# Performance work log

Hardware: AMD Instinct MI355X
Metric: run time of the kernel (lower is better)

Reference implementation:

```python
import jax, jax.numpy as jnp
import numpy as np

B, C, H, W = 2, 256, 32, 32
PK, CK = 256, 256


def setup_inputs() -> dict:
    key = jax.random.key(0)
    ks = jax.random.split(key, 9)
    s = 1.0 / np.sqrt(C)
    return {
        'x': jax.random.normal(ks[0], (B, C, H, W), jnp.float32),
        'primary_indices': jax.random.randint(ks[1], (B, PK), 0, B * H * W),
        'compare_indices': jax.random.randint(ks[2], (B, CK), 0, B * H * W),
        'pre_w': jax.random.uniform(ks[3], (3, C, C), jnp.float32, -s, s),
        'pre_b': jax.random.uniform(ks[4], (3, C), jnp.float32, -s, s),
        'post_w': jax.random.uniform(ks[5], (2, C, C), jnp.float32, -s, s),
        'post_b': jax.random.uniform(ks[6], (2, C), jnp.float32, -s, s),
        'post_out_w': jax.random.uniform(ks[7], (2, C), jnp.float32, -s, s),
        'post_out_b': jax.random.uniform(ks[8], (2,), jnp.float32, -s, s),
    }


def reference(x, primary_indices, compare_indices, pre_w, pre_b,
              post_w, post_b, post_out_w, post_out_b):
    # pre_compare: stack of 1x1 convs (c->c->c->c), ReLU between layers
    h = x
    for i in range(3):
        h = jnp.einsum('bchw,oc->bohw', h, pre_w[i]) + pre_b[i][None, :, None, None]
        if i < 2:
            h = jax.nn.relu(h)
    bs, c, hh, ww = h.shape
    # flatten to [bs*h*w, c] node features (matches torch transpose+reshape)
    flat = h.reshape(bs, c, hh * ww).transpose(0, 2, 1).reshape(bs * hh * ww, c)
    # gather primary / compare node features with global flat indices
    xp = flat[primary_indices.reshape(-1)].reshape(bs, -1, c).transpose(0, 2, 1)  # [b,c,pk]
    xc = flat[compare_indices.reshape(-1)].reshape(bs, -1, c).transpose(0, 2, 1)  # [b,c,ck]
    # broadcast pairwise squared difference -> [b,c,pk,ck]
    xx = (xp[:, :, :, None] - xc[:, :, None, :]) ** 2
    # post_compare: 1x1 conv stack c->c->c->2, ReLU between layers
    g = xx
    for i in range(2):
        g = jax.nn.relu(jnp.einsum('bcpq,oc->bopq', g, post_w[i]) + post_b[i][None, :, None, None])
    out = jnp.einsum('bcpq,oc->bopq', g, post_out_w) + post_out_b[None, :, None, None]
    return out  # [b, 2, pk, ck]
```

## Files before the change

### kernel.cpp

```cpp
#include <hip/hip_runtime.h>

typedef unsigned short u16;
typedef short bf16x8 __attribute__((ext_vector_type(8)));
typedef float f32x4 __attribute__((ext_vector_type(4)));
typedef u16 u16x4 __attribute__((ext_vector_type(4)));

__device__ __forceinline__ float b2f(u16 h) {
  unsigned u = ((unsigned)h) << 16;
  return __builtin_bit_cast(float, u);
}
__device__ __forceinline__ u16 f2b(float f) {
  return __builtin_bit_cast(u16, (__bf16)f);
}
__device__ __forceinline__ void gld_lds16(const void* g, void* l) {
  __builtin_amdgcn_global_load_lds(
      (__attribute__((address_space(1))) void*)(g),
      (__attribute__((address_space(3))) void*)(l), 16, 0, 0);
}

__global__ void dense_edge_prep(const float* __restrict__ x,
                                const float* __restrict__ pre_w,
                                const float* __restrict__ post_w,
                                u16* __restrict__ wb, u16* __restrict__ xt) {
  const int blk = blockIdx.x;
  const int t = threadIdx.x;
  if (blk < 160) {
    const int id = blk * 256 + t;
    const int layer = id >> 13;
    const int sid = id & 8191;
    const int m = sid >> 5;
    const int s8 = sid & 31;
    const float* src = (layer < 2) ? (post_w + layer * 65536)
                                   : (pre_w + (layer - 2) * 65536);
    u16* dst = wb + layer * 65536;
    f32x4 a = *(const f32x4*)(src + m * 256 + s8 * 8);
    f32x4 c = *(const f32x4*)(src + m * 256 + s8 * 8 + 4);
    bf16x8 o;
#pragma unroll
    for (int j = 0; j < 4; j++) o[j] = (short)f2b(a[j]);
#pragma unroll
    for (int j = 0; j < 4; j++) o[4 + j] = (short)f2b(c[j]);
    *(bf16x8*)(dst + (s8 * 256 + m) * 8) = o;
  } else {
    __shared__ float tile[32 * 65];
    const int xb = blk - 160;
    const int b = xb >> 7;
    const int ct = (xb >> 4) & 7;
    const int ht = xb & 15;
    const int c0 = ct * 32, hw0 = ht * 64;
#pragma unroll
    for (int rep = 0; rep < 8; rep++) {
      const int idx = rep * 256 + t;
      const int cl = idx >> 6, hl = idx & 63;
      tile[cl * 65 + hl] = x[(b * 256 + c0 + cl) * 1024 + hw0 + hl];
    }
    __syncthreads();
    const int hl = t >> 2, c8 = t & 3;
    bf16x8 o;
#pragma unroll
    for (int i = 0; i < 8; i++) o[i] = (short)f2b(tile[(c8 * 8 + i) * 65 + hl]);
    *(bf16x8*)(xt + (b * 1024 + hw0 + hl) * 256 + c0 + c8 * 8) = o;
  }
}

__global__ __launch_bounds__(256, 2) void dense_edge_pre(
    const u16* __restrict__ xt, const u16* __restrict__ wpre,
    const float* __restrict__ preb, u16* __restrict__ flat) {
  __shared__ u16 feat[2][2112];
  const int t = threadIdx.x;
  const int wv = t >> 6, ln = t & 63;
  const int nb = blockIdx.x * 8;
  const int q4 = ln >> 4, r15 = ln & 15;

  {
    const int s8 = t >> 3, nl = t & 7;
    gld_lds16(xt + (nb + nl) * 256 + s8 * 8, &feat[0][t * 8]);
  }
  __syncthreads();

#pragma unroll
  for (int l = 0; l < 3; l++) {
    const u16* wl = wpre + l * 65536;
    f32x4 acc[4];
    f32x4 zero = {0.f, 0.f, 0.f, 0.f};
#pragma unroll
    for (int mt = 0; mt < 4; mt++) acc[mt] = zero;
#pragma unroll
    for (int s = 0; s < 8; s++) {
      bf16x8 bv = *(const bf16x8*)(&feat[l & 1][((s * 4 + q4) * 8 + r15) * 8]);
#pragma unroll
      for (int mt = 0; mt < 4; mt++) {
        bf16x8 av = *(const bf16x8*)(wl + ((s * 4 + q4) * 256 + wv * 64 + mt * 16 + r15) * 8);
        acc[mt] = __builtin_amdgcn_mfma_f32_16x16x32_bf16(av, bv, acc[mt], 0, 0, 0);
      }
    }
    if (l < 2) {
#pragma unroll
      for (int mt = 0; mt < 4; mt++) {
        const int o = wv * 64 + mt * 16 + q4 * 4;
        f32x4 bb = *(const f32x4*)(preb + l * 256 + o);
        u16x4 pk;
#pragma unroll
        for (int r = 0; r < 4; r++) {
          float v = fmaxf(acc[mt][r] + bb[r], 0.f);
          pk[r] = f2b(v);
        }
        if (r15 < 8)
          *(u16x4*)(&feat[(l + 1) & 1][((o >> 3) * 8 + r15) * 8 + (o & 7)]) = pk;
      }
      __syncthreads();
    } else {
#pragma unroll
      for (int mt = 0; mt < 4; mt++) {
        const int o = wv * 64 + mt * 16 + q4 * 4;
        f32x4 bb = *(const f32x4*)(preb + 512 + o);
        u16x4 pk;
#pragma unroll
        for (int r = 0; r < 4; r++) pk[r] = f2b(acc[mt][r] + bb[r]);
        if (r15 < 8) *(u16x4*)(flat + (nb + r15) * 256 + o) = pk;
      }
    }
  }
}

#define NT 8
__global__ __launch_bounds__(512, 2) void dense_edge_main(
    const u16* __restrict__ flat, const int* __restrict__ pidx,
    const int* __restrict__ cidx, const u16* __restrict__ w1s,
    const u16* __restrict__ w2s, const float* __restrict__ b1,
    const float* __restrict__ b2, const float* __restrict__ w3,
    const float* __restrict__ b3, float* __restrict__ out) {
  __shared__ u16 xxbuf[2][16384];
  __shared__ u16 t1buf[2][16384];
  __shared__ u16 pstage[2048];
  __shared__ u16 qstage[2][2048];
  __shared__ float pbuf[2][8][2][64];

  const int t = threadIdx.x;
  const int wv = t >> 6;
  const int ln = t & 63;
  const int q4 = ln >> 4, r15 = ln & 15;
  const int blk = blockIdx.x;
  const int tile0 = blk * NT;
  const int b = tile0 >> 10;
  const int pt = (tile0 >> 5) & 31;
  const int qt0 = tile0 & 31;
  const int p0 = pt * 8;

  bf16x8 w1f[2][8], w2f[2][8];
#pragma unroll
  for (int s = 0; s < 8; s++)
#pragma unroll
    for (int mt = 0; mt < 2; mt++) {
      const int off = ((s * 4 + q4) * 256 + wv * 32 + mt * 16 + r15) * 8;
      w1f[mt][s] = *(const bf16x8*)(w1s + off);
      w2f[mt][s] = *(const bf16x8*)(w2s + off);
    }

  const int slot4 = (wv & 3) * 64 + ln;
  const int srow = slot4 & 7, scc = slot4 >> 3;
  if (wv < 4) {
    const int pn = pidx[b * 256 + p0 + srow];
    gld_lds16(flat + pn * 256 + scc * 8, &pstage[slot4 * 8]);
  } else {
    const int qn = cidx[b * 256 + qt0 * 8 + srow];
    gld_lds16(flat + qn * 256 + scc * 8, &qstage[0][slot4 * 8]);
  }
  int qn_pro = 0, qn_cur = 0;
  if (wv >= 4) {
    qn_pro = cidx[b * 256 + (qt0 + 1) * 8 + srow];
    qn_cur = cidx[b * 256 + (qt0 + 2) * 8 + srow];
  }
  __syncthreads();

  const int prow = ln >> 3, qrow = ln & 7;

  bf16x8 pa[4];
#pragma unroll
  for (int i = 0; i < 4; i++)
    pa[i] = *(const bf16x8*)(&pstage[((wv * 4 + i) * 8 + prow) * 8]);

  auto do_xx = [&](int jx) {
    const u16* qs = qstage[jx & 1];
    u16* xb = xxbuf[jx & 1];
#pragma unroll
    for (int i = 0; i < 4; i++) {
      const int cc = wv * 4 + i;
      bf16x8 av = pa[i];
      bf16x8 bv = *(const bf16x8*)(&qs[(cc * 8 + qrow) * 8]);
      bf16x8 ov;
#pragma unroll
      for (int jj = 0; jj < 8; jj++) {
        float d = b2f((u16)av[jj]) - b2f((u16)bv[jj]);
        ov[jj] = (short)f2b(d * d);
      }
      *(bf16x8*)(&xb[(cc * 64 + ln) * 8]) = ov;
    }
  };

  auto do_g1 = [&](int jg) {
    const u16* xb = xxbuf[jg & 1];
    f32x4 acc[2][4];
    {
      f32x4 zero = {0.f, 0.f, 0.f, 0.f};
#pragma unroll
      for (int mt = 0; mt < 2; mt++)
#pragma unroll
        for (int nt = 0; nt < 4; nt++) acc[mt][nt] = zero;
    }
    __builtin_amdgcn_s_setprio(1);
#pragma unroll
    for (int s = 0; s < 8; s++) {
      bf16x8 bfr[4];
#pragma unroll
      for (int nt = 0; nt < 4; nt++)
        bfr[nt] = *(const bf16x8*)(xb + ((s * 4 + q4) * 64 + nt * 16 + r15) * 8);
#pragma unroll
      for (int mt = 0; mt < 2; mt++)
#pragma unroll
        for (int nt = 0; nt < 4; nt++)
          acc[mt][nt] = __builtin_amdgcn_mfma_f32_16x16x32_bf16(w1f[mt][s], bfr[nt], acc[mt][nt], 0, 0, 0);
    }
    __builtin_amdgcn_s_setprio(0);
#pragma unroll
    for (int mt = 0; mt < 2; mt++) {
      const int o = wv * 32 + mt * 16 + q4 * 4;
      f32x4 bb = *(const f32x4*)(b1 + o);
#pragma unroll
      for (int nt = 0; nt < 4; nt++) {
        const int nn = nt * 16 + r15;
        u16x4 pk;
#pragma unroll
        for (int r = 0; r < 4; r++) {
          float v = fmaxf(acc[mt][nt][r] + bb[r], 0.f);
          pk[r] = f2b(v);
        }
        *(u16x4*)(&t1buf[jg & 1][((o >> 3) * 64 + nn) * 8 + (o & 7)]) = pk;
      }
    }
  };

  auto do_g2 = [&](int jg) {
    const u16* tb = t1buf[jg & 1];
    f32x4 acc[2][4];
    {
      f32x4 zero = {0.f, 0.f, 0.f, 0.f};
#pragma unroll
      for (int mt = 0; mt < 2; mt++)
#pragma unroll
        for (int nt = 0; nt < 4; nt++) acc[mt][nt] = zero;
    }
    __builtin_amdgcn_s_setprio(1);
#pragma unroll
    for (int s = 0; s < 8; s++) {
      bf16x8 bfr[4];
#pragma unroll
      for (int nt = 0; nt < 4; nt++)
        bfr[nt] = *(const bf16x8*)(tb + ((s * 4 + q4) * 64 + nt * 16 + r15) * 8);
#pragma unroll
      for (int mt = 0; mt < 2; mt++)
#pragma unroll
        for (int nt = 0; nt < 4; nt++)
          acc[mt][nt] = __builtin_amdgcn_mfma_f32_16x16x32_bf16(w2f[mt][s], bfr[nt], acc[mt][nt], 0, 0, 0);
    }
    __builtin_amdgcn_s_setprio(0);
    float part[2][4] = {{0.f, 0.f, 0.f, 0.f}, {0.f, 0.f, 0.f, 0.f}};
#pragma unroll
    for (int mt = 0; mt < 2; mt++) {
      const int o = wv * 32 + mt * 16 + q4 * 4;
      f32x4 bb = *(const f32x4*)(b2 + o);
      f32x4 w3a = *(const f32x4*)(w3 + o);
      f32x4 w3b = *(const f32x4*)(w3 + 256 + o);
#pragma unroll
      for (int nt = 0; nt < 4; nt++) {
#pragma unroll
        for (int r = 0; r < 4; r++) {
          float v = fmaxf(acc[mt][nt][r] + bb[r], 0.f);
          part[0][nt] += v * w3a[r];
          part[1][nt] += v * w3b[r];
        }
      }
    }
#pragma unroll
    for (int o3 = 0; o3 < 2; o3++)
#pragma unroll
      for (int nt = 0; nt < 4; nt++) {
        part[o3][nt] += __shfl_xor(part[o3][nt], 16, 64);
        part[o3][nt] += __shfl_xor(part[o3][nt], 32, 64);
      }
    if (q4 == 0) {
#pragma unroll
      for (int o3 = 0; o3 < 2; o3++)
#pragma unroll
        for (int nt = 0; nt < 4; nt++)
          pbuf[jg & 1][wv][o3][nt * 16 + r15] = part[o3][nt];
    }
  };

  do_xx(0);
  if (wv >= 4) gld_lds16(flat + qn_pro * 256 + scc * 8, &qstage[1][slot4 * 8]);
  __syncthreads();

#pragma unroll 1
  for (int j = 0; j <= NT; j++) {
    if (j >= 2 && t < 128) {
      const int jo = j - 2;
      const int o3 = t >> 6;
      const int n = t & 63;
      float v = b3[o3];
#pragma unroll
      for (int k = 0; k < 8; k++) v += pbuf[jo & 1][k][o3][n];
      out[((b * 2 + o3) * 256 + p0 + (n >> 3)) * 256 + (qt0 + jo) * 8 + (n & 7)] = v;
    }
    if (j < NT - 2 && wv >= 4) {
      gld_lds16(flat + qn_cur * 256 + scc * 8, &qstage[j & 1][slot4 * 8]);
      if (j < NT - 3) qn_cur = cidx[b * 256 + (qt0 + j + 3) * 8 + srow];
    }
    if (wv & 4) {
      if (j < NT - 1) do_xx(j + 1);
      if (j > 0) do_g2(j - 1);
      if (j < NT) do_g1(j);
    } else {
      if (j < NT) do_g1(j);
      if (j > 0) do_g2(j - 1);
      if (j < NT - 1) do_xx(j + 1);
    }
    __syncthreads();
  }

  if (t < 128) {
    const int jo = NT - 1;
    const int o3 = t >> 6;
    const int n = t & 63;
    float v = b3[o3];
#pragma unroll
    for (int k = 0; k < 8; k++) v += pbuf[jo & 1][k][o3][n];
    out[((b * 2 + o3) * 256 + p0 + (n >> 3)) * 256 + (qt0 + jo) * 8 + (n & 7)] = v;
  }
}

extern "C" void kernel_launch(void* const* d_in, const int* in_sizes, int n_in,
                              void* d_out, int out_size, void* d_ws, size_t ws_size,
                              hipStream_t stream) {
  (void)in_sizes; (void)n_in; (void)out_size; (void)ws_size;
  const float* x          = (const float*)d_in[0];
  const int*   pidx       = (const int*)d_in[1];
  const int*   cidx       = (const int*)d_in[2];
  const float* pre_w      = (const float*)d_in[3];
  const float* pre_b      = (const float*)d_in[4];
  const float* post_w     = (const float*)d_in[5];
  const float* post_b     = (const float*)d_in[6];
  const float* post_out_w = (const float*)d_in[7];
  const float* post_out_b = (const float*)d_in[8];
  float* out = (float*)d_out;

  u16* ws   = (u16*)d_ws;
  u16* wb   = ws;
  u16* w1s  = wb;
  u16* w2s  = wb + 65536;
  u16* wpre = wb + 131072;
  u16* xt   = ws + 327680;
  u16* flat = ws + 851968;

  dense_edge_prep<<<416, 256, 0, stream>>>(x, pre_w, post_w, wb, xt);
  dense_edge_pre<<<256, 256, 0, stream>>>(xt, wpre, pre_b, flat);
  dense_edge_main<<<256, 512, 0, stream>>>(flat, pidx, cidx, w1s, w2s,
                                           post_b, post_b + 256,
                                           post_out_w, post_out_b, out);
}
```

Measured before the change: 119.6 us.

## Specialize waves into layer-1 producers and layer-2 consumers with per-layer weight registers

Splits the eight waves into two groups. Four producer waves compute the squared differences and the first post-conv GEMM. The other four consumer waves run the second GEMM, the output reduction and the global stores. Each wave now holds only one layer's weights, covering 64 output channels instead of 32 per layer. This halves the weight register footprint per output and removes duplicate weight loading across layers. The trade-off is possible load imbalance between the groups, since the producer waves also do the xx computation, and more accumulator registers per wave.

```diff
diff --git a/kernel.cpp b/kernel.cpp
--- a/kernel.cpp
+++ b/kernel.cpp
@@ -134,12 +134,14 @@
   __shared__ u16 t1buf[2][16384];
   __shared__ u16 pstage[2048];
   __shared__ u16 qstage[2][2048];
-  __shared__ float pbuf[2][8][2][64];
+  __shared__ float pbuf[2][4][2][64];
 
   const int t = threadIdx.x;
   const int wv = t >> 6;
   const int ln = t & 63;
   const int q4 = ln >> 4, r15 = ln & 15;
+  const bool prod = wv < 4;
+  const int cw = wv & 3;
   const int blk = blockIdx.x;
   const int tile0 = blk * NT;
   const int b = tile0 >> 10;
@@ -147,46 +149,37 @@
   const int qt0 = tile0 & 31;
   const int p0 = pt * 8;
 
-  bf16x8 w1f[2][8], w2f[2][8];
+  const u16* wsrc = prod ? w1s : w2s;
+  bf16x8 af_w[4][8];
 #pragma unroll
   for (int s = 0; s < 8; s++)
 #pragma unroll
-    for (int mt = 0; mt < 2; mt++) {
-      const int off = ((s * 4 + q4) * 256 + wv * 32 + mt * 16 + r15) * 8;
-      w1f[mt][s] = *(const bf16x8*)(w1s + off);
-      w2f[mt][s] = *(const bf16x8*)(w2s + off);
-    }
-
-  const int slot4 = (wv & 3) * 64 + ln;
+    for (int mt = 0; mt < 4; mt++)
+      af_w[mt][s] = *(const bf16x8*)(wsrc + ((s * 4 + q4) * 256 + cw * 64 + mt * 16 + r15) * 8);
+
+  const int slot4 = cw * 64 + ln;
   const int srow = slot4 & 7, scc = slot4 >> 3;
-  if (wv < 4) {
+  int qn_pro = 0, qn_cur = 0;
+  if (prod) {
     const int pn = pidx[b * 256 + p0 + srow];
     gld_lds16(flat + pn * 256 + scc * 8, &pstage[slot4 * 8]);
+    qn_pro = cidx[b * 256 + (qt0 + 1) * 8 + srow];
+    qn_cur = cidx[b * 256 + (qt0 + 2) * 8 + srow];
   } else {
     const int qn = cidx[b * 256 + qt0 * 8 + srow];
     gld_lds16(flat + qn * 256 + scc * 8, &qstage[0][slot4 * 8]);
   }
-  int qn_pro = 0, qn_cur = 0;
-  if (wv >= 4) {
-    qn_pro = cidx[b * 256 + (qt0 + 1) * 8 + srow];
-    qn_cur = cidx[b * 256 + (qt0 + 2) * 8 + srow];
-  }
   __syncthreads();
 
   const int prow = ln >> 3, qrow = ln & 7;
-
-  bf16x8 pa[4];
-#pragma unroll
-  for (int i = 0; i < 4; i++)
-    pa[i] = *(const bf16x8*)(&pstage[((wv * 4 + i) * 8 + prow) * 8]);
 
   auto do_xx = [&](int jx) {
     const u16* qs = qstage[jx & 1];
     u16* xb = xxbuf[jx & 1];
 #pragma unroll
-    for (int i = 0; i < 4; i++) {
-      const int cc = wv * 4 + i;
-      bf16x8 av = pa[i];
+    for (int i = 0; i < 8; i++) {
+      const int cc = cw * 8 + i;
+      bf16x8 av = *(const bf16x8*)(&pstage[(cc * 8 + prow) * 8]);
       bf16x8 bv = *(const bf16x8*)(&qs[(cc * 8 + qrow) * 8]);
       bf16x8 ov;
 #pragma unroll
@@ -200,11 +193,11 @@
 
   auto do_g1 = [&](int jg) {
     const u16* xb = xxbuf[jg & 1];
-    f32x4 acc[2][4];
+    f32x4 acc[4][4];
     {
       f32x4 zero = {0.f, 0.f, 0.f, 0.f};
 #pragma unroll
-      for (int mt = 0; mt < 2; mt++)
+      for (int mt = 0; mt < 4; mt++)
 #pragma unroll
         for (int nt = 0; nt < 4; nt++) acc[mt][nt] = zero;
     }
@@ -216,15 +209,15 @@
       for (int nt = 0; nt < 4; nt++)
         bfr[nt] = *(const bf16x8*)(xb + ((s * 4 + q4) * 64 + nt * 16 + r15) * 8);
 #pragma unroll
-      for (int mt = 0; mt < 2; mt++)
+      for (int mt = 0; mt < 4; mt++)
 #pragma unroll
         for (int nt = 0; nt < 4; nt++)
-          acc[mt][nt] = __builtin_amdgcn_mfma_f32_16x16x32_bf16(w1f[mt][s], bfr[nt], acc[mt][nt], 0, 0, 0);
+          acc[mt][nt] = __builtin_amdgcn_mfma_f32_16x16x32_bf16(af_w[mt][s], bfr[nt], acc[mt][nt], 0, 0, 0);
     }
     __builtin_amdgcn_s_setprio(0);
 #pragma unroll
-    for (int mt = 0; mt < 2; mt++) {
-      const int o = wv * 32 + mt * 16 + q4 * 4;
+    for (int mt = 0; mt < 4; mt++) {
+      const int o = cw * 64 + mt * 16 + q4 * 4;
       f32x4 bb = *(const f32x4*)(b1 + o);
 #pragma unroll
       for (int nt = 0; nt < 4; nt++) {
@@ -242,11 +235,11 @@
 
   auto do_g2 = [&](int jg) {
     const u16* tb = t1buf[jg & 1];
-    f32x4 acc[2][4];
+    f32x4 acc[4][4];
     {
       f32x4 zero = {0.f, 0.f, 0.f, 0.f};
 #pragma unroll
-      for (int mt = 0; mt < 2; mt++)
+      for (int mt = 0; mt < 4; mt++)
 #pragma unroll
         for (int nt = 0; nt < 4; nt++) acc[mt][nt] = zero;
     }
@@ -258,16 +251,16 @@
       for (int nt = 0; nt < 4; nt++)
         bfr[nt] = *(const bf16x8*)(tb + ((s * 4 + q4) * 64 + nt * 16 + r15) * 8);
 #pragma unroll
-      for (int mt = 0; mt < 2; mt++)
+      for (int mt = 0; mt < 4; mt++)
 #pragma unroll
         for (int nt = 0; nt < 4; nt++)
-          acc[mt][nt] = __builtin_amdgcn_mfma_f32_16x16x32_bf16(w2f[mt][s], bfr[nt], acc[mt][nt], 0, 0, 0);
+          acc[mt][nt] = __builtin_amdgcn_mfma_f32_16x16x32_bf16(af_w[mt][s], bfr[nt], acc[mt][nt], 0, 0, 0);
     }
     __builtin_amdgcn_s_setprio(0);
     float part[2][4] = {{0.f, 0.f, 0.f, 0.f}, {0.f, 0.f, 0.f, 0.f}};
 #pragma unroll
-    for (int mt = 0; mt < 2; mt++) {
-      const int o = wv * 32 + mt * 16 + q4 * 4;
+    for (int mt = 0; mt < 4; mt++) {
+      const int o = cw * 64 + mt * 16 + q4 * 4;
       f32x4 bb = *(const f32x4*)(b2 + o);
       f32x4 w3a = *(const f32x4*)(w3 + o);
       f32x4 w3b = *(const f32x4*)(w3 + 256 + o);
@@ -293,49 +286,54 @@
       for (int o3 = 0; o3 < 2; o3++)
 #pragma unroll
         for (int nt = 0; nt < 4; nt++)
-          pbuf[jg & 1][wv][o3][nt * 16 + r15] = part[o3][nt];
+          pbuf[jg & 1][cw][o3][nt * 16 + r15] = part[o3][nt];
     }
   };
 
-  do_xx(0);
-  if (wv >= 4) gld_lds16(flat + qn_pro * 256 + scc * 8, &qstage[1][slot4 * 8]);
+  if (prod) {
+    do_xx(0);
+    gld_lds16(flat + qn_pro * 256 + scc * 8, &qstage[1][slot4 * 8]);
+  }
   __syncthreads();
 
 #pragma unroll 1
   for (int j = 0; j <= NT; j++) {
-    if (j >= 2 && t < 128) {
-      const int jo = j - 2;
-      const int o3 = t >> 6;
-      const int n = t & 63;
+    if (prod) {
+      if (j < NT - 2) {
+        gld_lds16(flat + qn_cur * 256 + scc * 8, &qstage[j & 1][slot4 * 8]);
+        if (j < NT - 3) qn_cur = cidx[b * 256 + (qt0 + j + 3) * 8 + srow];
+      }
+      if (j < NT) do_g1(j);
+      if (j < NT - 1) do_xx(j + 1);
+    } else {
+      if (j >= 2) {
+        const int jo = j - 2;
+        const int tt = t & 255;
+        if (tt < 128) {
+          const int o3 = tt >> 6;
+          const int n = tt & 63;
+          float v = b3[o3];
+#pragma unroll
+          for (int k = 0; k < 4; k++) v += pbuf[jo & 1][k][o3][n];
+          out[((b * 2 + o3) * 256 + p0 + (n >> 3)) * 256 + (qt0 + jo) * 8 + (n & 7)] = v;
+        }
+      }
+      if (j > 0) do_g2(j - 1);
+    }
+    __syncthreads();
+  }
+
+  if (!prod) {
+    const int jo = NT - 1;
+    const int tt = t & 255;
+    if (tt < 128) {
+      const int o3 = tt >> 6;
+      const int n = tt & 63;
       float v = b3[o3];
 #pragma unroll
-      for (int k = 0; k < 8; k++) v += pbuf[jo & 1][k][o3][n];
+      for (int k = 0; k < 4; k++) v += pbuf[jo & 1][k][o3][n];
       out[((b * 2 + o3) * 256 + p0 + (n >> 3)) * 256 + (qt0 + jo) * 8 + (n & 7)] = v;
     }
-    if (j < NT - 2 && wv >= 4) {
-      gld_lds16(flat + qn_cur * 256 + scc * 8, &qstage[j & 1][slot4 * 8]);
-      if (j < NT - 3) qn_cur = cidx[b * 256 + (qt0 + j + 3) * 8 + srow];
-    }
-    if (wv & 4) {
-      if (j < NT - 1) do_xx(j + 1);
-      if (j > 0) do_g2(j - 1);
-      if (j < NT) do_g1(j);
-    } else {
-      if (j < NT) do_g1(j);
-      if (j > 0) do_g2(j - 1);
-      if (j < NT - 1) do_xx(j + 1);
-    }
-    __syncthreads();
-  }
-
-  if (t < 128) {
-    const int jo = NT - 1;
-    const int o3 = t >> 6;
-    const int n = t & 63;
-    float v = b3[o3];
-#pragma unroll
-    for (int k = 0; k < 8; k++) v += pbuf[jo & 1][k][o3][n];
-    out[((b * 2 + o3) * 256 + p0 + (n >> 3)) * 256 + (qt0 + jo) * 8 + (n & 7)] = v;
   }
 }
 
```

After: 128.5 us. 1.07x slower.

## Fuse prep and pre-conv kernels, converting weights and input on the fly

Applied to the files above, without the earlier changes.

Merges the separate prep kernel (fp32->bf16 weight packing and x transpose) into the pre-conv kernel. The pre-conv now reads fp32 x directly, transposes it through LDS, and converts fp32 pre_w to bf16 per MFMA operand. Post weights are still packed by extra blocks within the same launch. This removes one kernel launch and the xt/wpre workspace round trip. The cost is that every block rereads and reconverts the fp32 pre weights, doubling weight bytes per load. It also flips which waves take the reversed xx/g2/g1 ordering in the main kernel.

```diff
diff --git a/kernel.cpp b/kernel.cpp
--- a/kernel.cpp
+++ b/kernel.cpp
@@ -12,75 +12,71 @@
 __device__ __forceinline__ u16 f2b(float f) {
   return __builtin_bit_cast(u16, (__bf16)f);
 }
+__device__ __forceinline__ bf16x8 cvt8(f32x4 a, f32x4 b) {
+  bf16x8 o;
+#pragma unroll
+  for (int k = 0; k < 4; k++) {
+    o[k] = (short)f2b(a[k]);
+    o[4 + k] = (short)f2b(b[k]);
+  }
+  return o;
+}
 __device__ __forceinline__ void gld_lds16(const void* g, void* l) {
   __builtin_amdgcn_global_load_lds(
       (__attribute__((address_space(1))) void*)(g),
       (__attribute__((address_space(3))) void*)(l), 16, 0, 0);
 }
 
-__global__ void dense_edge_prep(const float* __restrict__ x,
-                                const float* __restrict__ pre_w,
-                                const float* __restrict__ post_w,
-                                u16* __restrict__ wb, u16* __restrict__ xt) {
+__global__ __launch_bounds__(256, 2) void dense_edge_pre2(
+    const float* __restrict__ x, const float* __restrict__ pre_w,
+    const float* __restrict__ preb, const float* __restrict__ post_w,
+    u16* __restrict__ wb, u16* __restrict__ flat) {
+  const int t = threadIdx.x;
   const int blk = blockIdx.x;
-  const int t = threadIdx.x;
-  if (blk < 160) {
-    const int id = blk * 256 + t;
+  if (blk >= 256) {
+    const int id = (blk - 256) * 256 + t;
     const int layer = id >> 13;
     const int sid = id & 8191;
     const int m = sid >> 5;
     const int s8 = sid & 31;
-    const float* src = (layer < 2) ? (post_w + layer * 65536)
-                                   : (pre_w + (layer - 2) * 65536);
+    const float* src = post_w + layer * 65536;
     u16* dst = wb + layer * 65536;
     f32x4 a = *(const f32x4*)(src + m * 256 + s8 * 8);
     f32x4 c = *(const f32x4*)(src + m * 256 + s8 * 8 + 4);
-    bf16x8 o;
-#pragma unroll
-    for (int j = 0; j < 4; j++) o[j] = (short)f2b(a[j]);
-#pragma unroll
-    for (int j = 0; j < 4; j++) o[4 + j] = (short)f2b(c[j]);
-    *(bf16x8*)(dst + (s8 * 256 + m) * 8) = o;
-  } else {
-    __shared__ float tile[32 * 65];
-    const int xb = blk - 160;
-    const int b = xb >> 7;
-    const int ct = (xb >> 4) & 7;
-    const int ht = xb & 15;
-    const int c0 = ct * 32, hw0 = ht * 64;
-#pragma unroll
-    for (int rep = 0; rep < 8; rep++) {
-      const int idx = rep * 256 + t;
-      const int cl = idx >> 6, hl = idx & 63;
-      tile[cl * 65 + hl] = x[(b * 256 + c0 + cl) * 1024 + hw0 + hl];
-    }
-    __syncthreads();
-    const int hl = t >> 2, c8 = t & 3;
-    bf16x8 o;
-#pragma unroll
-    for (int i = 0; i < 8; i++) o[i] = (short)f2b(tile[(c8 * 8 + i) * 65 + hl]);
-    *(bf16x8*)(xt + (b * 1024 + hw0 + hl) * 256 + c0 + c8 * 8) = o;
-  }
-}
-
-__global__ __launch_bounds__(256, 2) void dense_edge_pre(
-    const u16* __restrict__ xt, const u16* __restrict__ wpre,
-    const float* __restrict__ preb, u16* __restrict__ flat) {
+    *(bf16x8*)(dst + (s8 * 256 + m) * 8) = cvt8(a, c);
+    return;
+  }
+
+  __shared__ __align__(16) float tile[8 * 260];
   __shared__ u16 feat[2][2112];
-  const int t = threadIdx.x;
+
   const int wv = t >> 6, ln = t & 63;
-  const int nb = blockIdx.x * 8;
+  const int nb = blk * 8;
+  const int b = nb >> 10, hw0 = nb & 1023;
   const int q4 = ln >> 4, r15 = ln & 15;
 
   {
-    const int s8 = t >> 3, nl = t & 7;
-    gld_lds16(xt + (nb + nl) * 256 + s8 * 8, &feat[0][t * 8]);
+    const float* src = x + (b * 256 + t) * 1024 + hw0;
+    f32x4 v0 = *(const f32x4*)src;
+    f32x4 v1 = *(const f32x4*)(src + 4);
+#pragma unroll
+    for (int e = 0; e < 4; e++) {
+      tile[e * 260 + t] = v0[e];
+      tile[(4 + e) * 260 + t] = v1[e];
+    }
   }
   __syncthreads();
+  {
+    const float* p = tile + (t & 7) * 260 + (t >> 3) * 8;
+    f32x4 a = *(const f32x4*)p;
+    f32x4 c4 = *(const f32x4*)(p + 4);
+    *(bf16x8*)(&feat[0][t * 8]) = cvt8(a, c4);
+  }
+  __syncthreads();
 
 #pragma unroll
   for (int l = 0; l < 3; l++) {
-    const u16* wl = wpre + l * 65536;
+    const float* wl = pre_w + l * 65536;
     f32x4 acc[4];
     f32x4 zero = {0.f, 0.f, 0.f, 0.f};
 #pragma unroll
@@ -90,8 +86,10 @@
       bf16x8 bv = *(const bf16x8*)(&feat[l & 1][((s * 4 + q4) * 8 + r15) * 8]);
 #pragma unroll
       for (int mt = 0; mt < 4; mt++) {
-        bf16x8 av = *(const bf16x8*)(wl + ((s * 4 + q4) * 256 + wv * 64 + mt * 16 + r15) * 8);
-        acc[mt] = __builtin_amdgcn_mfma_f32_16x16x32_bf16(av, bv, acc[mt], 0, 0, 0);
+        const float* wp = wl + (wv * 64 + mt * 16 + r15) * 256 + (s * 4 + q4) * 8;
+        f32x4 wa = *(const f32x4*)wp;
+        f32x4 wc = *(const f32x4*)(wp + 4);
+        acc[mt] = __builtin_amdgcn_mfma_f32_16x16x32_bf16(cvt8(wa, wc), bv, acc[mt], 0, 0, 0);
       }
     }
     if (l < 2) {
@@ -316,7 +314,7 @@
       gld_lds16(flat + qn_cur * 256 + scc * 8, &qstage[j & 1][slot4 * 8]);
       if (j < NT - 3) qn_cur = cidx[b * 256 + (qt0 + j + 3) * 8 + srow];
     }
-    if (wv & 4) {
+    if (wv & 1) {
       if (j < NT - 1) do_xx(j + 1);
       if (j > 0) do_g2(j - 1);
       if (j < NT) do_g1(j);
@@ -355,15 +353,11 @@
   float* out = (float*)d_out;
 
   u16* ws   = (u16*)d_ws;
-  u16* wb   = ws;
-  u16* w1s  = wb;
-  u16* w2s  = wb + 65536;
-  u16* wpre = wb + 131072;
-  u16* xt   = ws + 327680;
-  u16* flat = ws + 851968;
-
-  dense_edge_prep<<<416, 256, 0, stream>>>(x, pre_w, post_w, wb, xt);
-  dense_edge_pre<<<256, 256, 0, stream>>>(xt, wpre, pre_b, flat);
+  u16* w1s  = ws;
+  u16* w2s  = ws + 65536;
+  u16* flat = ws + 131072;
+
+  dense_edge_pre2<<<320, 256, 0, stream>>>(x, pre_w, pre_b, post_w, ws, flat);
   dense_edge_main<<<256, 512, 0, stream>>>(flat, pidx, cidx, w1s, w2s,
                                            post_b, post_b + 256,
                                            post_out_w, post_out_b, out);
```

After: 137.4 us. 14.9% more time.
